# Kernel optimization log

Hardware: AMD Instinct MI355X
Metric: run time of the kernel (lower is better)

## Reference

```python
import jax, jax.numpy as jnp
import numpy as np

N_NODES = 100000
N_EDGES = 1600000
IN_DIM = 256
OUT_DIM = 64


def setup_inputs() -> dict:
    key = jax.random.key(0)
    k1, k2, k3 = jax.random.split(key, 3)
    inputs = jax.random.normal(k1, (N_NODES, IN_DIM), dtype=jnp.float32)
    edge_index = jax.random.randint(k2, (2, N_EDGES), 0, N_NODES, dtype=jnp.int64)
    # Xavier-uniform weight as in nn.init.xavier_uniform_
    limit = float(np.sqrt(6.0 / (IN_DIM + OUT_DIM)))
    weight = jax.random.uniform(k3, (IN_DIM, OUT_DIM), minval=-limit, maxval=limit, dtype=jnp.float32)
    return {"inputs": inputs, "edge_index": edge_index, "weight": weight}


def reference(inputs, edge_index, weight):
    # Dense projection: [N, out_dim]
    x = inputs @ weight
    # Sparse adjacency matmul: out[r] = sum_{(r,c) in edges} x[c]
    rows, cols = edge_index[0], edge_index[1]
    agg = jax.ops.segment_sum(x[cols], rows, num_segments=inputs.shape[0])
    return jax.nn.sigmoid(agg)
```

## Files before the change

### kernel.cpp

```cpp
#include <hip/hip_runtime.h>
#include <hip/hip_fp16.h>
#include <math.h>

#define N_NODES 100000
#define N_EDGES 1600000
#define IN_DIM 256
#define OUT_DIM 64

#define NB 512
#define RPB 196
#define BCAP 3712
#define CAP 24
#define CHUNK_E 4096
#define NBIN_BLK ((N_EDGES + CHUNK_E - 1) / CHUNK_E)

#define X_OFF         0UL
#define BP_OFF        12800000UL
#define WIMG_OFF      20500000UL
#define BCUR_OFF      20600000UL

typedef short bf16x8 __attribute__((ext_vector_type(8)));
typedef float f32x4 __attribute__((ext_vector_type(4)));

__global__ __launch_bounds__(256) void convert_weight(const float* __restrict__ w,
                                                      ushort* __restrict__ img,
                                                      int* __restrict__ bcur) {
    const int g = blockIdx.x * 256 + threadIdx.x;
    if (g < NB) bcur[g] = 0;
    const int j = g & 7, l = (g >> 3) & 63, ts = g >> 9;
    const int s = ts & 7, t = ts >> 3;
    const int k = s * 32 + (l >> 4) * 8 + j;
    const int c = t * 16 + (l & 15);
    const float v = w[k * OUT_DIM + c];
    const unsigned b = __float_as_uint(v);
    const float r = v - __uint_as_float(b & 0xFFFF0000u);
    img[(ts * 2 + 0) * 512 + l * 8 + j] = (ushort)(b >> 16);
    img[(ts * 2 + 1) * 512 + l * 8 + j] = (ushort)(__float_as_uint(r) >> 16);
}

__global__ __launch_bounds__(256) void gemm_mfma(const float* __restrict__ inputs,
                                                 const ushort* __restrict__ wimg,
                                                 __half* __restrict__ x) {
    __shared__ ushort lds[32768];
    const int tid = threadIdx.x;

    #pragma unroll
    for (int i = 0; i < 16; ++i) {
        const int c = tid + i * 256;
        *(int4*)(lds + c * 8) = *(const int4*)(wimg + c * 8);
    }
    __syncthreads();

    const int wv = tid >> 6, l = tid & 63;
    const int rbase = blockIdx.x * 64 + wv * 16;
    const int arow_idx = rbase + (l & 15);
    const int row_c = arow_idx < N_NODES ? arow_idx : N_NODES - 1;
    const float* arow = inputs + (size_t)row_c * IN_DIM;
    const int koff = (l >> 4) * 8;

    bf16x8 ah[8], al[8];
    #pragma unroll
    for (int s = 0; s < 8; ++s) {
        const float4 p = *(const float4*)(arow + s * 32 + koff);
        const float4 q = *(const float4*)(arow + s * 32 + koff + 4);
        const float v[8] = {p.x, p.y, p.z, p.w, q.x, q.y, q.z, q.w};
        #pragma unroll
        for (int j = 0; j < 8; ++j) {
            const unsigned b = __float_as_uint(v[j]);
            const float r = v[j] - __uint_as_float(b & 0xFFFF0000u);
            ah[s][j] = (short)(b >> 16);
            al[s][j] = (short)(__float_as_uint(r) >> 16);
        }
    }

    f32x4 acc[4];
    #pragma unroll
    for (int t = 0; t < 4; ++t) acc[t] = (f32x4){0.f, 0.f, 0.f, 0.f};

    const bf16x8* b8 = (const bf16x8*)lds;
    #pragma unroll
    for (int t = 0; t < 4; ++t) {
        #pragma unroll
        for (int s = 0; s < 8; ++s) {
            const bf16x8 bh = b8[((t * 8 + s) * 2 + 0) * 64 + l];
            const bf16x8 blo = b8[((t * 8 + s) * 2 + 1) * 64 + l];
            acc[t] = __builtin_amdgcn_mfma_f32_16x16x32_bf16(ah[s], bh, acc[t], 0, 0, 0);
            acc[t] = __builtin_amdgcn_mfma_f32_16x16x32_bf16(al[s], bh, acc[t], 0, 0, 0);
            acc[t] = __builtin_amdgcn_mfma_f32_16x16x32_bf16(ah[s], blo, acc[t], 0, 0, 0);
        }
    }

    const int mbase = rbase + (l >> 4) * 4;
    #pragma unroll
    for (int reg = 0; reg < 4; ++reg) {
        const int row = mbase + reg;
        if (row < N_NODES) {
            #pragma unroll
            for (int t = 0; t < 4; ++t)
                x[(size_t)row * OUT_DIM + t * 16 + (l & 15)] = __float2half(acc[t][reg]);
        }
    }
}

__global__ __launch_bounds__(256) void bin_kernel(const int* __restrict__ rows,
                                                  const int* __restrict__ cols,
                                                  int* __restrict__ bcur,
                                                  int* __restrict__ bp) {
    __shared__ int lbuf[NB * CAP];
    __shared__ int lcnt[NB], ltot[NB], lbase[NB];
    const int tid = threadIdx.x;
    lcnt[tid] = 0; lcnt[tid + 256] = 0;
    __syncthreads();

    const int base = blockIdx.x * CHUNK_E;
    #pragma unroll
    for (int g = 0; g < 4; ++g) {
        const int e = base + (g * 256 + tid) * 4;
        if (e < N_EDGES) {
            const int4 r4 = *(const int4*)(rows + e);
            const int4 c4 = *(const int4*)(cols + e);
            const int rr[4] = {r4.x, r4.y, r4.z, r4.w};
            const int cc[4] = {c4.x, c4.y, c4.z, c4.w};
            #pragma unroll
            for (int u = 0; u < 4; ++u) {
                const int r = rr[u];
                const int b = r / RPB;
                const int pack = ((r - b * RPB) << 17) | cc[u];
                const int p = atomicAdd(&lcnt[b], 1);
                if (p < CAP) {
                    lbuf[b * CAP + p] = pack;
                } else {
                    const int gp = atomicAdd(&bcur[b], 1);
                    if (gp < BCAP) bp[b * BCAP + gp] = pack;
                }
            }
        }
    }
    __syncthreads();
    #pragma unroll
    for (int q = 0; q < 2; ++q) {
        const int b = tid + q * 256;
        const int tot = min(lcnt[b], CAP);
        ltot[b] = tot;
        lbase[b] = atomicAdd(&bcur[b], tot);
    }
    __syncthreads();
    #pragma unroll
    for (int k = 0; k < 64; ++k) {
        const int b = (k << 3) + (tid >> 5);
        const int i = tid & 31;
        if (i < ltot[b]) {
            const int gp = lbase[b] + i;
            if (gp < BCAP) bp[b * BCAP + gp] = lbuf[b * CAP + i];
        }
    }
}

__global__ __launch_bounds__(1024) void aggregate_kernel(const int* __restrict__ bp,
                                                         const int* __restrict__ bcur,
                                                         const __half* __restrict__ x,
                                                         float* __restrict__ out) {
    __shared__ int ebuf[BCAP];
    __shared__ int sbuf[BCAP];
    __shared__ int hist[RPB];
    __shared__ int roff[RPB + 1];
    __shared__ int cur[RPB];
    __shared__ int sc[256], sc2[256];
    const int b = blockIdx.x, t = threadIdx.x;
    const int n = min(bcur[b], BCAP);
    const int* bb = bp + b * BCAP;

    if (t < RPB) hist[t] = 0;
    __syncthreads();

    const int4* bb4 = (const int4*)bb;
    for (int i = t; i * 4 + 3 < n; i += 1024) {
        const int4 v = bb4[i];
        *(int4*)(ebuf + i * 4) = v;
        atomicAdd(&hist[v.x >> 17], 1);
        atomicAdd(&hist[v.y >> 17], 1);
        atomicAdd(&hist[v.z >> 17], 1);
        atomicAdd(&hist[v.w >> 17], 1);
    }
    {
        const int i = (n & ~3) + t;
        if (i < n) {
            const int v = bb[i];
            ebuf[i] = v;
            atomicAdd(&hist[v >> 17], 1);
        }
    }
    __syncthreads();

    if (t < 256) sc[t] = (t < RPB) ? hist[t] : 0;
    __syncthreads();
    int* src = sc; int* dst = sc2;
    for (int off = 1; off < 256; off <<= 1) {
        if (t < 256) dst[t] = src[t] + ((t >= off) ? src[t - off] : 0);
        __syncthreads();
        int* tmp = src; src = dst; dst = tmp;
    }
    if (t < RPB) { const int e = src[t] - hist[t]; roff[t] = e; cur[t] = e; }
    if (t == 0) roff[RPB] = n;
    __syncthreads();

    for (int i = t; i < n; i += 1024) {
        const int v = ebuf[i];
        const int p = atomicAdd(&cur[v >> 17], 1);
        sbuf[p] = v & 0x1FFFF;
    }
    __syncthreads();

    const int w = t >> 6, lane = t & 63;
    const int g = lane >> 4;
    const int s = lane & 15;
    const __half* xs = x + s * 4;

    for (int rl = w; rl < RPB; rl += 16) {
        const int row = b * RPB + rl;
        if (row >= N_NODES) break;
        const int start = roff[rl];
        const int end = roff[rl + 1];
        float a0 = 0.f, a1 = 0.f, a2 = 0.f, a3 = 0.f;
        int j = start;
        for (; j + 15 < end; j += 16) {
            int c[4];
            #pragma unroll
            for (int u = 0; u < 4; ++u) c[u] = sbuf[j + u * 4 + g];
            #pragma unroll
            for (int u = 0; u < 4; ++u) {
                const uint2 d = *(const uint2*)(xs + (size_t)c[u] * OUT_DIM);
                const float2 f0 = __half22float2(*(const __half2*)&d.x);
                const float2 f1 = __half22float2(*(const __half2*)&d.y);
                a0 += f0.x; a1 += f0.y; a2 += f1.x; a3 += f1.y;
            }
        }
        #pragma unroll
        for (int u = 0; u < 4; ++u) {
            const int ej = j + u * 4 + g;
            if (ej < end) {
                const int cc = sbuf[ej];
                const uint2 d = *(const uint2*)(xs + (size_t)cc * OUT_DIM);
                const float2 f0 = __half22float2(*(const __half2*)&d.x);
                const float2 f1 = __half22float2(*(const __half2*)&d.y);
                a0 += f0.x; a1 += f0.y; a2 += f1.x; a3 += f1.y;
            }
        }
        a0 += __shfl_xor(a0, 16); a0 += __shfl_xor(a0, 32);
        a1 += __shfl_xor(a1, 16); a1 += __shfl_xor(a1, 32);
        a2 += __shfl_xor(a2, 16); a2 += __shfl_xor(a2, 32);
        a3 += __shfl_xor(a3, 16); a3 += __shfl_xor(a3, 32);

        if (lane < 16) {
            float4 o;
            o.x = 1.f / (1.f + __expf(-a0));
            o.y = 1.f / (1.f + __expf(-a1));
            o.z = 1.f / (1.f + __expf(-a2));
            o.w = 1.f / (1.f + __expf(-a3));
            *(float4*)(out + (size_t)row * OUT_DIM + s * 4) = o;
        }
    }
}

extern "C" void kernel_launch(void* const* d_in, const int* in_sizes, int n_in,
                              void* d_out, int out_size, void* d_ws, size_t ws_size,
                              hipStream_t stream) {
    const float* inputs = (const float*)d_in[0];
    const int* edge_index = (const int*)d_in[1];
    const float* weight = (const float*)d_in[2];
    float* out = (float*)d_out;

    char* ws = (char*)d_ws;
    __half* x        = (__half*)(ws + X_OFF);
    int* bp          = (int*)(ws + BP_OFF);
    ushort* wimg     = (ushort*)(ws + WIMG_OFF);
    int* bcur        = (int*)(ws + BCUR_OFF);

    const int* rows = edge_index;
    const int* cols = edge_index + N_EDGES;

    convert_weight<<<64, 256, 0, stream>>>(weight, wimg, bcur);
    bin_kernel<<<NBIN_BLK, 256, 0, stream>>>(rows, cols, bcur, bp);
    gemm_mfma<<<(N_NODES + 63) / 64, 256, 0, stream>>>(inputs, wimg, x);
    aggregate_kernel<<<NB, 1024, 0, stream>>>(bp, bcur, x, out);
}
```

Before: 234.2 us.

## Fuse bin and GEMM kernels into one launch; widen aggregate gathers to 16B

Merges the edge binning kernel and the MFMA projection GEMM into one launch, using block-index ranges to dispatch and a shared 64KB LDS buffer, so the two independent stages can overlap and one launch gap is removed. In the aggregation kernel each lane now loads 8 halves (16 bytes) per neighbour instead of 4, with 8 lanes covering a row, and the loop is simplified into a single guarded loop over 32-edge strides. The larger LDS allocation may reduce occupancy for the bin blocks, and the per-element guard adds branches in the gather loop.

```diff
diff --git a/kernel.cpp b/kernel.cpp
--- a/kernel.cpp
+++ b/kernel.cpp
@@ -13,6 +13,7 @@
 #define CAP 24
 #define CHUNK_E 4096
 #define NBIN_BLK ((N_EDGES + CHUNK_E - 1) / CHUNK_E)
+#define NGEMM_BLK ((N_NODES + 63) / 64)
 
 #define X_OFF         0UL
 #define BP_OFF        12800000UL
@@ -38,10 +39,11 @@
     img[(ts * 2 + 1) * 512 + l * 8 + j] = (ushort)(__float_as_uint(r) >> 16);
 }
 
-__global__ __launch_bounds__(256) void gemm_mfma(const float* __restrict__ inputs,
-                                                 const ushort* __restrict__ wimg,
-                                                 __half* __restrict__ x) {
-    __shared__ ushort lds[32768];
+__device__ __forceinline__ void gemm_body(char* smem, int bid,
+                                          const float* __restrict__ inputs,
+                                          const ushort* __restrict__ wimg,
+                                          __half* __restrict__ x) {
+    ushort* lds = (ushort*)smem;
     const int tid = threadIdx.x;
 
     #pragma unroll
@@ -52,7 +54,7 @@
     __syncthreads();
 
     const int wv = tid >> 6, l = tid & 63;
-    const int rbase = blockIdx.x * 64 + wv * 16;
+    const int rbase = bid * 64 + wv * 16;
     const int arow_idx = rbase + (l & 15);
     const int row_c = arow_idx < N_NODES ? arow_idx : N_NODES - 1;
     const float* arow = inputs + (size_t)row_c * IN_DIM;
@@ -102,17 +104,20 @@
     }
 }
 
-__global__ __launch_bounds__(256) void bin_kernel(const int* __restrict__ rows,
-                                                  const int* __restrict__ cols,
-                                                  int* __restrict__ bcur,
-                                                  int* __restrict__ bp) {
-    __shared__ int lbuf[NB * CAP];
-    __shared__ int lcnt[NB], ltot[NB], lbase[NB];
+__device__ __forceinline__ void bin_body(char* smem, int bid,
+                                         const int* __restrict__ rows,
+                                         const int* __restrict__ cols,
+                                         int* __restrict__ bcur,
+                                         int* __restrict__ bp) {
+    int* lbuf  = (int*)smem;
+    int* lcnt  = (int*)(smem + NB * CAP * 4);
+    int* ltot  = lcnt + NB;
+    int* lbase = ltot + NB;
     const int tid = threadIdx.x;
     lcnt[tid] = 0; lcnt[tid + 256] = 0;
     __syncthreads();
 
-    const int base = blockIdx.x * CHUNK_E;
+    const int base = bid * CHUNK_E;
     #pragma unroll
     for (int g = 0; g < 4; ++g) {
         const int e = base + (g * 256 + tid) * 4;
@@ -156,6 +161,20 @@
     }
 }
 
+__global__ __launch_bounds__(256) void fused_gemm_bin(const float* __restrict__ inputs,
+                                                      const ushort* __restrict__ wimg,
+                                                      __half* __restrict__ x,
+                                                      const int* __restrict__ rows,
+                                                      const int* __restrict__ cols,
+                                                      int* __restrict__ bcur,
+                                                      int* __restrict__ bp) {
+    __shared__ __align__(16) char smem[65536];
+    if (blockIdx.x < NBIN_BLK)
+        bin_body(smem, blockIdx.x, rows, cols, bcur, bp);
+    else
+        gemm_body(smem, blockIdx.x - NBIN_BLK, inputs, wimg, x);
+}
+
 __global__ __launch_bounds__(1024) void aggregate_kernel(const int* __restrict__ bp,
                                                          const int* __restrict__ bcur,
                                                          const __half* __restrict__ x,
@@ -212,52 +231,55 @@
     __syncthreads();
 
     const int w = t >> 6, lane = t & 63;
-    const int g = lane >> 4;
-    const int s = lane & 15;
-    const __half* xs = x + s * 4;
+    const int g = lane >> 3;
+    const int s = lane & 7;
+    const __half* xs = x + s * 8;
 
     for (int rl = w; rl < RPB; rl += 16) {
         const int row = b * RPB + rl;
         if (row >= N_NODES) break;
         const int start = roff[rl];
         const int end = roff[rl + 1];
-        float a0 = 0.f, a1 = 0.f, a2 = 0.f, a3 = 0.f;
-        int j = start;
-        for (; j + 15 < end; j += 16) {
-            int c[4];
-            #pragma unroll
-            for (int u = 0; u < 4; ++u) c[u] = sbuf[j + u * 4 + g];
+        float a[8];
+        #pragma unroll
+        for (int q = 0; q < 8; ++q) a[q] = 0.f;
+
+        for (int j = start; j < end; j += 32) {
             #pragma unroll
             for (int u = 0; u < 4; ++u) {
-                const uint2 d = *(const uint2*)(xs + (size_t)c[u] * OUT_DIM);
-                const float2 f0 = __half22float2(*(const __half2*)&d.x);
-                const float2 f1 = __half22float2(*(const __half2*)&d.y);
-                a0 += f0.x; a1 += f0.y; a2 += f1.x; a3 += f1.y;
+                const int ej = j + u * 8 + g;
+                if (ej < end) {
+                    const int cc = sbuf[ej];
+                    const uint4 d = *(const uint4*)(xs + (size_t)cc * OUT_DIM);
+                    const __half2* h2 = (const __half2*)&d;
+                    #pragma unroll
+                    for (int q = 0; q < 4; ++q) {
+                        const float2 f = __half22float2(h2[q]);
+                        a[2 * q] += f.x; a[2 * q + 1] += f.y;
+                    }
+                }
             }
         }
         #pragma unroll
-        for (int u = 0; u < 4; ++u) {
-            const int ej = j + u * 4 + g;
-            if (ej < end) {
-                const int cc = sbuf[ej];
-                const uint2 d = *(const uint2*)(xs + (size_t)cc * OUT_DIM);
-                const float2 f0 = __half22float2(*(const __half2*)&d.x);
-                const float2 f1 = __half22float2(*(const __half2*)&d.y);
-                a0 += f0.x; a1 += f0.y; a2 += f1.x; a3 += f1.y;
-            }
-        }
-        a0 += __shfl_xor(a0, 16); a0 += __shfl_xor(a0, 32);
-        a1 += __shfl_xor(a1, 16); a1 += __shfl_xor(a1, 32);
-        a2 += __shfl_xor(a2, 16); a2 += __shfl_xor(a2, 32);
-        a3 += __shfl_xor(a3, 16); a3 += __shfl_xor(a3, 32);
-
-        if (lane < 16) {
-            float4 o;
-            o.x = 1.f / (1.f + __expf(-a0));
-            o.y = 1.f / (1.f + __expf(-a1));
-            o.z = 1.f / (1.f + __expf(-a2));
-            o.w = 1.f / (1.f + __expf(-a3));
-            *(float4*)(out + (size_t)row * OUT_DIM + s * 4) = o;
+        for (int q = 0; q < 8; ++q) {
+            a[q] += __shfl_xor(a[q], 8);
+            a[q] += __shfl_xor(a[q], 16);
+            a[q] += __shfl_xor(a[q], 32);
+        }
+
+        if (lane < 8) {
+            float4 o0, o1;
+            o0.x = 1.f / (1.f + __expf(-a[0]));
+            o0.y = 1.f / (1.f + __expf(-a[1]));
+            o0.z = 1.f / (1.f + __expf(-a[2]));
+            o0.w = 1.f / (1.f + __expf(-a[3]));
+            o1.x = 1.f / (1.f + __expf(-a[4]));
+            o1.y = 1.f / (1.f + __expf(-a[5]));
+            o1.z = 1.f / (1.f + __expf(-a[6]));
+            o1.w = 1.f / (1.f + __expf(-a[7]));
+            float* op = out + (size_t)row * OUT_DIM + s * 8;
+            *(float4*)op = o0;
+            *(float4*)(op + 4) = o1;
         }
     }
 }
@@ -280,7 +302,7 @@
     const int* cols = edge_index + N_EDGES;
 
     convert_weight<<<64, 256, 0, stream>>>(weight, wimg, bcur);
-    bin_kernel<<<NBIN_BLK, 256, 0, stream>>>(rows, cols, bcur, bp);
-    gemm_mfma<<<(N_NODES + 63) / 64, 256, 0, stream>>>(inputs, wimg, x);
+    fused_gemm_bin<<<NBIN_BLK + NGEMM_BLK, 256, 0, stream>>>(inputs, wimg, x,
+                                                             rows, cols, bcur, bp);
     aggregate_kernel<<<NB, 1024, 0, stream>>>(bp, bcur, x, out);
 }
```

New measurement: 231.3 us. No clear change (-1.2%).
